# Optimization experiments

Measured on AMD Instinct MI355X. Metric: run time of the kernel, lower is better.

Reference implementation:

```python
import jax, jax.numpy as jnp
import numpy as np
from jax import lax

# --- block geometry (matches init_kwargs) ---
B = 8
DIM = 192
HEADS = 6
KEY_DIM = DIM // HEADS  # 32, attn_ratio=1 so d == key_dim and dh == DIM
HX, WX = 32, 32         # search region
HZ, WZ = 16, 16         # template region
T = 1                   # template_number
L = HX * WX + T * HZ * WZ  # 1280 tokens
MLP_HIDDEN = int(DIM * 4.0)
BN_EPS = 1e-5


def _build_bias_idx():
    """Replicates Attention.__init__ global_att=True bias-index construction.
    Unique-offset ids may be permuted vs torch dict-insertion order, which is an
    equivalent reparameterization of the (randomly initialized) bias table."""
    g = np.stack(np.meshgrid(np.arange(HX), np.arange(WX), indexing='ij'), -1).reshape(-1, 2)
    pts = [g]
    for i in range(T):
        r = np.arange(HX + HZ * i, WX + WZ * (i + 1))
        g2 = np.stack(np.meshgrid(r, r, indexing='ij'), -1).reshape(-1, 2)
        pts.append(g2)
    p = np.concatenate(pts, 0)                      # (L, 2)
    off = np.abs(p[:, None, :] - p[None, :, :])     # (L, L, 2)
    key = off[:, :, 0].astype(np.int64) * 4096 + off[:, :, 1]
    uniq, inv = np.unique(key, return_inverse=True)
    return inv.reshape(L, L).astype(np.int32), int(len(uniq))


def setup_inputs() -> dict:
    key = jax.random.key(0)
    ks = jax.random.split(key, 16)
    idx_np, n_off = _build_bias_idx()
    s = 0.02
    return {
        'xz': jax.random.normal(ks[0], (B, L, DIM), jnp.float32),
        'bias_idx': jnp.asarray(idx_np),
        'ln1_g': jnp.ones((DIM,), jnp.float32),
        'ln1_b': jnp.zeros((DIM,), jnp.float32),
        'wqkv': jax.random.normal(ks[1], (DIM, 3 * DIM), jnp.float32) * s,
        'bqkv': jnp.zeros((3 * DIM,), jnp.float32),
        'wproj': jax.random.normal(ks[2], (DIM, DIM), jnp.float32) * s,
        'bproj': jnp.zeros((DIM,), jnp.float32),
        'bias_table': jax.random.normal(ks[3], (HEADS, n_off), jnp.float32) * 0.1,
        'conv_w': jax.random.normal(ks[4], (3, 3, 1, DIM), jnp.float32) * 0.1,  # depthwise HWIO
        'bn_scale': jnp.ones((DIM,), jnp.float32) + jax.random.normal(ks[5], (DIM,), jnp.float32) * 0.01,
        'bn_bias': jax.random.normal(ks[6], (DIM,), jnp.float32) * 0.01,
        'ln2_g': jnp.ones((DIM,), jnp.float32),
        'ln2_b': jnp.zeros((DIM,), jnp.float32),
        'w1': jax.random.normal(ks[7], (DIM, MLP_HIDDEN), jnp.float32) * s,
        'b1': jnp.zeros((MLP_HIDDEN,), jnp.float32),
        'w2': jax.random.normal(ks[8], (MLP_HIDDEN, DIM), jnp.float32) * s,
        'b2': jnp.zeros((DIM,), jnp.float32),
    }


def _layernorm(x, g, b, eps=1e-5):
    mu = jnp.mean(x, -1, keepdims=True)
    var = jnp.mean(jnp.square(x - mu), -1, keepdims=True)
    return (x - mu) * lax.rsqrt(var + eps) * g + b


def reference(xz, bias_idx, ln1_g, ln1_b, wqkv, bqkv, wproj, bproj, bias_table,
              conv_w, bn_scale, bn_bias, ln2_g, ln2_b, w1, b1, w2, b2):
    Bn, N, D = xz.shape
    scale = KEY_DIM ** -0.5
    # --- Attention (LeViT-style with gathered relative-position bias) ---
    h = _layernorm(xz, ln1_g, ln1_b)
    qkv = (h @ wqkv + bqkv).reshape(Bn, N, HEADS, 3 * KEY_DIM)
    q, k, v = jnp.split(qkv, 3, axis=3)            # each (B, N, H, key_dim)
    bias = bias_table[:, bias_idx]                  # (H, N, N) gather
    attn = jnp.einsum('bnhd,bmhd->bhnm', q, k) * scale + bias
    attn = jax.nn.softmax(attn, axis=-1)
    o = jnp.einsum('bhnm,bmhd->bnhd', attn, v).reshape(Bn, N, D)
    xm = xz + o @ wproj + bproj
    # --- depthwise local conv (Conv2d_BN, BN folded to scale/bias) per segment ---
    segs = []
    start = 0
    for (Hh, Ww) in [(HX, WX)] + [(HZ, WZ)] * T:
        xc = xm[:, start:start + Hh * Ww, :].reshape(Bn, Hh, Ww, D)
        xc = lax.conv_general_dilated(
            xc, conv_w, window_strides=(1, 1), padding='SAME',
            dimension_numbers=('NHWC', 'HWIO', 'NHWC'), feature_group_count=D)
        xc = xc * bn_scale + bn_bias
        segs.append(xc.reshape(Bn, Hh * Ww, D))
        start += Hh * Ww
    xm = jnp.concatenate(segs, axis=1)
    # --- MLP with pre-LN (exact GELU, matching nn.GELU default) ---
    m = _layernorm(xm, ln2_g, ln2_b)
    m = jax.nn.gelu(m @ w1 + b1, approximate=False) @ w2 + b2
    return xm + m
```

## Files before the change

kernel.cpp:

```cpp
#include <hip/hip_runtime.h>
#include <hip/hip_bf16.h>

#define BATCH 8
#define LTOK 1280
#define DIMC 192
#define HEADS 6
#define KD 32
#define HID 768
#define NROWS (BATCH*LTOK)

typedef short s16x8 __attribute__((ext_vector_type(8)));
typedef float f32x4 __attribute__((ext_vector_type(4)));
typedef unsigned short u16;

#define QS (0.17677669529663687f * 1.4426950408889634f)
#define L2E 1.4426950408889634f

__device__ __forceinline__ u16 f2bf(float x) {
    unsigned u = __float_as_uint(x);
    u = (u + 0x7FFFu + ((u >> 16) & 1u)) >> 16;
    return (u16)u;
}
__device__ __forceinline__ float bflo(unsigned u) { return __uint_as_float(u << 16); }
__device__ __forceinline__ float bfhi(unsigned u) { return __uint_as_float(u & 0xffff0000u); }
__device__ __forceinline__ float fexp2(float x) { float r; asm("v_exp_f32 %0, %1" : "=v"(r) : "v"(x)); return r; }
__device__ __forceinline__ float frcp(float x)  { float r; asm("v_rcp_f32 %0, %1" : "=v"(r) : "v"(x)); return r; }

__global__ __launch_bounds__(256) void ln_kernel(const float* __restrict__ x,
                                                 const float* __restrict__ g,
                                                 const float* __restrict__ b,
                                                 u16* __restrict__ y) {
    int row = blockIdx.x * 4 + (threadIdx.x >> 6);
    int lane = threadIdx.x & 63;
    const float* xr = x + (size_t)row * DIMC;
    float v0 = xr[lane], v1 = xr[lane + 64], v2 = xr[lane + 128];
    float s = v0 + v1 + v2;
    float ss = v0 * v0 + v1 * v1 + v2 * v2;
    #pragma unroll
    for (int off = 32; off; off >>= 1) {
        s  += __shfl_xor(s, off);
        ss += __shfl_xor(ss, off);
    }
    float mu  = s * (1.0f / DIMC);
    float var = ss * (1.0f / DIMC) - mu * mu;
    float inv = rsqrtf(var + 1e-5f);
    u16* yr = y + (size_t)row * DIMC;
    yr[lane]       = f2bf((v0 - mu) * inv * g[lane]       + b[lane]);
    yr[lane + 64]  = f2bf((v1 - mu) * inv * g[lane + 64]  + b[lane + 64]);
    yr[lane + 128] = f2bf((v2 - mu) * inv * g[lane + 128] + b[lane + 128]);
}

__global__ __launch_bounds__(256) void pre_kernel(const float* w0, const float* w1,
                                                  const float* w2, const float* w3,
                                                  u16* o0, u16* o1, u16* o2, u16* o3,
                                                  const int* __restrict__ bidx,
                                                  const float* __restrict__ btab,
                                                  int n_off, u16* __restrict__ bm) {
    __shared__ float s[16][17];
    int f = blockIdx.x;
    if (f >= 1728) {
        size_t flat = (size_t)(f - 1728) * 1024 + (size_t)threadIdx.x * 4;
        int4 iv = *(const int4*)(bidx + flat);
        #pragma unroll
        for (int h = 0; h < HEADS; ++h) {
            const float* tab = btab + (size_t)h * n_off;
            ushort4 o;
            o.x = f2bf(tab[iv.x] * L2E);
            o.y = f2bf(tab[iv.y] * L2E);
            o.z = f2bf(tab[iv.z] * L2E);
            o.w = f2bf(tab[iv.w] * L2E);
            *(ushort4*)(bm + (size_t)h * (LTOK * LTOK) + flat) = o;
        }
        return;
    }
    const float* in; u16* out; int K, N, tn, tk;
    if (f < 432)       { in = w0; out = o0; K = 192; N = 576; int r = f;        tn = r % 36; tk = r / 36; }
    else if (f < 576)  { in = w1; out = o1; K = 192; N = 192; int r = f - 432;  tn = r % 12; tk = r / 12; }
    else if (f < 1152) { in = w2; out = o2; K = 192; N = 768; int r = f - 576;  tn = r % 48; tk = r / 48; }
    else               { in = w3; out = o3; K = 768; N = 192; int r = f - 1152; tn = r % 12; tk = r / 12; }
    int tx = threadIdx.x & 15, ty = threadIdx.x >> 4;
    s[ty][tx] = in[(size_t)(tk * 16 + ty) * N + tn * 16 + tx];
    __syncthreads();
    out[(size_t)(tn * 16 + ty) * K + tk * 16 + tx] = f2bf(s[tx][ty]);
}

template<int ACT, int RES, int OBF, int QKV, int K, int MTILE>
__global__ __launch_bounds__(256) void gemm_mfma(const u16* __restrict__ A,
                                                 const u16* __restrict__ Wt,
                                                 const float* __restrict__ bias,
                                                 const float* __restrict__ R,
                                                 void* __restrict__ Cp,
                                                 u16* __restrict__ qb,
                                                 u16* __restrict__ kp,
                                                 u16* __restrict__ vp,
                                                 int N) {
    constexpr int SUB = MTILE / 64;
    int tid = threadIdx.x;
    int L = tid & 63, w = tid >> 6;
    int r = L & 15, g = L >> 4;
    int m0 = blockIdx.y * MTILE + w * (16 * SUB);
    int n0 = blockIdx.x * 64;

    f32x4 acc[SUB][4] = {};
    const u16* Ab = A + (size_t)(m0 + r) * K + g * 8;
    const u16* Wb = Wt + (size_t)(n0 + r) * K + g * 8;
    #pragma unroll 6
    for (int k0 = 0; k0 < K; k0 += 32) {
        s16x8 af[SUB];
        #pragma unroll
        for (int mi = 0; mi < SUB; ++mi)
            af[mi] = *(const s16x8*)(Ab + (size_t)mi * 16 * K + k0);
        #pragma unroll
        for (int nn = 0; nn < 4; ++nn) {
            s16x8 bf = *(const s16x8*)(Wb + (size_t)nn * 16 * K + k0);
            #pragma unroll
            for (int mi = 0; mi < SUB; ++mi)
                acc[mi][nn] = __builtin_amdgcn_mfma_f32_16x16x32_bf16(af[mi], bf, acc[mi][nn], 0, 0, 0);
        }
    }

    #pragma unroll
    for (int mi = 0; mi < SUB; ++mi)
    #pragma unroll
    for (int nn = 0; nn < 4; ++nn) {
        int cb = n0 + nn * 16;
        #pragma unroll
        for (int i = 0; i < 4; ++i) {
            int row = m0 + mi * 16 + g * 4 + i;
            float v = acc[mi][nn][i] + bias[cb + r];
            if (QKV) {
                int h  = cb / 96, c0 = cb % 96;
                int reg = c0 >> 5;
                if (reg == 0) {
                    v *= QS;
                    qb[(size_t)row * DIMC + h * 32 + (c0 & 31) + r] = f2bf(v);
                } else {
                    int b_ = row / LTOK, t = row - b_ * LTOK;
                    int T = t >> 5, it = t & 31;
                    int d = (c0 & 31) + r;
                    if (reg == 1) {
                        int which = (it >> 2) & 1;
                        int ik = ((it >> 3) << 2) | (it & 3);
                        int Lk = ((d >> 3) << 4) + ik;
                        kp[((size_t)(b_ * HEADS + h) * 40 + T) * 1024 + which * 512 + Lk * 8 + (d & 7)] = f2bf(v);
                    } else {
                        int Lv = ((it >> 3) << 4) + (d & 15);
                        vp[((size_t)(b_ * HEADS + h) * 40 + T) * 1024 + (d >> 4) * 512 + Lv * 8 + (it & 7)] = f2bf(v);
                    }
                }
            } else {
                if (ACT == 1) {
                    float u = v;
                    float y = 0.7978845608028654f * (u + 0.044715f * u * u * u);
                    float e2 = fexp2(y * 2.885390081777927f);
                    v = u - u * frcp(e2 + 1.0f);
                }
                if (RES) v += R[(size_t)row * N + cb + r];
                if (OBF) ((u16*)Cp)[(size_t)row * N + cb + r] = f2bf(v);
                else     ((float*)Cp)[(size_t)row * N + cb + r] = v;
            }
        }
    }
}

__global__ __launch_bounds__(256) void attn_mfma(const u16* __restrict__ qb,
                                                 const u16* __restrict__ kp,
                                                 const u16* __restrict__ vp,
                                                 const u16* __restrict__ bm,
                                                 u16* __restrict__ ob) {
    __shared__ __align__(16) u16 kvs[2][2][2][1024];
    int tid = threadIdx.x;
    int L = tid & 63, w = tid >> 6;
    int r = L & 15, g = L >> 4;
    int L8 = L * 8;

    int bid = blockIdx.x;
    int work = (bid & 7) * 60 + (bid >> 3);
    int bp = work & 3;
    int hq = work >> 2;
    int qt = (hq % 20) * 4 + w;
    int h  = hq / 20;
    int b0 = bp * 2;

    s16x8 qfr[2];
    qfr[0] = *(const s16x8*)(qb + (size_t)(b0 * LTOK + qt * 16 + r) * DIMC + h * 32 + g * 8);
    qfr[1] = *(const s16x8*)(qb + (size_t)((b0 + 1) * LTOK + qt * 16 + r) * DIMC + h * 32 + g * 8);

    int sbi = w >> 1, skv = w & 1;
    const u16* gsrc = (skv ? vp : kp) + ((size_t)((b0 + sbi) * HEADS + h) * 40) * 1024 + L8;
    u16* lds0 = &kvs[0][sbi][skv][L8];
    u16* lds1 = &kvs[1][sbi][skv][L8];

    const u16* bmr = bm + ((size_t)h * LTOK + qt * 16 + r) * LTOK + g * 8;

    f32x4 acc0[2] = {}, acc1[2] = {};
    float lsum[2] = {0.f, 0.f};

    int4 sA = *(const int4*)(gsrc);
    int4 sB = *(const int4*)(gsrc + 512);
    int4 bvn = *(const int4*)(bmr);
    *(int4*)lds0 = sA;
    *(int4*)(lds0 + 512) = sB;
    __syncthreads();

    #pragma unroll 1
    for (int T = 0; T < 40; ++T) {
        int buf = T & 1;
        if (T < 39) {
            sA = *(const int4*)(gsrc + (size_t)(T + 1) * 1024);
            sB = *(const int4*)(gsrc + (size_t)(T + 1) * 1024 + 512);
        }
        int4 bv = bvn;
        if (T < 39) bvn = *(const int4*)(bmr + (size_t)(T + 1) * 32);

        f32x4 z0, z1;
        z0[0] = bflo(bv.x); z0[1] = bfhi(bv.x); z0[2] = bflo(bv.y); z0[3] = bfhi(bv.y);
        z1[0] = bflo(bv.z); z1[1] = bfhi(bv.z); z1[2] = bflo(bv.w); z1[3] = bfhi(bv.w);

        #pragma unroll
        for (int bi = 0; bi < 2; ++bi) {
            s16x8 kf0 = *(const s16x8*)&kvs[buf][bi][0][L8];
            s16x8 kf1 = *(const s16x8*)&kvs[buf][bi][0][512 + L8];
            f32x4 s0 = __builtin_amdgcn_mfma_f32_16x16x32_bf16(kf0, qfr[bi], z0, 0, 0, 0);
            f32x4 s1 = __builtin_amdgcn_mfma_f32_16x16x32_bf16(kf1, qfr[bi], z1, 0, 0, 0);
            float p[8];
            #pragma unroll
            for (int j = 0; j < 4; ++j) p[j] = fexp2(s0[j]);
            #pragma unroll
            for (int j = 0; j < 4; ++j) p[4 + j] = fexp2(s1[j]);
            lsum[bi] += ((p[0] + p[1]) + (p[2] + p[3])) + ((p[4] + p[5]) + (p[6] + p[7]));
            union { unsigned u[4]; s16x8 v; } pbu;
            #pragma unroll
            for (int j = 0; j < 4; ++j)
                asm("v_cvt_pk_bf16_f32 %0, %1, %2" : "=v"(pbu.u[j]) : "v"(p[2 * j]), "v"(p[2 * j + 1]));
            s16x8 v0 = *(const s16x8*)&kvs[buf][bi][1][L8];
            s16x8 v1 = *(const s16x8*)&kvs[buf][bi][1][512 + L8];
            acc0[bi] = __builtin_amdgcn_mfma_f32_16x16x32_bf16(pbu.v, v0, acc0[bi], 0, 0, 0);
            acc1[bi] = __builtin_amdgcn_mfma_f32_16x16x32_bf16(pbu.v, v1, acc1[bi], 0, 0, 0);
        }

        if (T < 39) {
            u16* ld = (T & 1) ? lds0 : lds1;
            *(int4*)ld = sA;
            *(int4*)(ld + 512) = sB;
        }
        __syncthreads();
    }

    #pragma unroll
    for (int bi = 0; bi < 2; ++bi) {
        float lr = lsum[bi];
        lr += __shfl_xor(lr, 16);
        lr += __shfl_xor(lr, 32);
        int b = b0 + bi;
        #pragma unroll
        for (int i = 0; i < 4; ++i) {
            float linv = frcp(__shfl(lr, 4 * g + i));
            size_t orow = (size_t)(b * LTOK + qt * 16 + 4 * g + i) * DIMC + h * 32 + r;
            ob[orow]      = f2bf(acc0[bi][i] * linv);
            ob[orow + 16] = f2bf(acc1[bi][i] * linv);
        }
    }
}

__global__ __launch_bounds__(256) void conv_bn_kernel(const float* __restrict__ xm,
                                                      const float* __restrict__ w,
                                                      const float* __restrict__ scale,
                                                      const float* __restrict__ bias,
                                                      float* __restrict__ out) {
    int idx = blockIdx.x * 256 + threadIdx.x;
    int cc = idx % 48, p = idx / 48;
    int c = cc * 4;
    int b = p / LTOK, t = p - b * LTOK;
    int H, W, base, y, x;
    if (t < 1024) { H = 32; W = 32; base = 0;    y = t >> 5;            x = t & 31; }
    else          { H = 16; W = 16; base = 1024; int tt = t - 1024; y = tt >> 4; x = tt & 15; }
    float4 acc = {0.f, 0.f, 0.f, 0.f};
    #pragma unroll
    for (int ky = 0; ky < 3; ++ky) {
        int yy = y + ky - 1;
        if (yy < 0 || yy >= H) continue;
        #pragma unroll
        for (int kx = 0; kx < 3; ++kx) {
            int xx = x + kx - 1;
            if (xx < 0 || xx >= W) continue;
            float4 wv = *(const float4*)(w + (ky * 3 + kx) * DIMC + c);
            float4 xv = *(const float4*)(xm + (size_t)(b * LTOK + base + yy * W + xx) * DIMC + c);
            acc.x += wv.x * xv.x; acc.y += wv.y * xv.y;
            acc.z += wv.z * xv.z; acc.w += wv.w * xv.w;
        }
    }
    float4 sv = *(const float4*)(scale + c);
    float4 bv = *(const float4*)(bias + c);
    float4 o;
    o.x = acc.x * sv.x + bv.x; o.y = acc.y * sv.y + bv.y;
    o.z = acc.z * sv.z + bv.z; o.w = acc.w * sv.w + bv.w;
    *(float4*)(out + (size_t)(b * LTOK + t) * DIMC + c) = o;
}

extern "C" void kernel_launch(void* const* d_in, const int* in_sizes, int n_in,
                              void* d_out, int out_size, void* d_ws, size_t ws_size,
                              hipStream_t stream) {
    const float* xz       = (const float*)d_in[0];
    const int*   bidx     = (const int*)  d_in[1];
    const float* ln1_g    = (const float*)d_in[2];
    const float* ln1_b    = (const float*)d_in[3];
    const float* wqkv     = (const float*)d_in[4];
    const float* bqkv     = (const float*)d_in[5];
    const float* wproj    = (const float*)d_in[6];
    const float* bproj    = (const float*)d_in[7];
    const float* btab     = (const float*)d_in[8];
    const float* conv_w   = (const float*)d_in[9];
    const float* bn_scale = (const float*)d_in[10];
    const float* bn_bias  = (const float*)d_in[11];
    const float* ln2_g    = (const float*)d_in[12];
    const float* ln2_b    = (const float*)d_in[13];
    const float* w1       = (const float*)d_in[14];
    const float* b1       = (const float*)d_in[15];
    const float* w2       = (const float*)d_in[16];
    const float* b2       = (const float*)d_in[17];
    int n_off = in_sizes[8] / HEADS;
    float* out = (float*)d_out;

    char* wsb = (char*)d_ws;
    u16*  hbuf   = (u16*)(wsb + 0);
    u16*  ob     = (u16*)(wsb + 0);
    u16*  wqkvT  = (u16*)(wsb + 3932160);
    u16*  wprojT = (u16*)(wsb + 4153344);
    u16*  w1T    = (u16*)(wsb + 4227072);
    u16*  w2T    = (u16*)(wsb + 4521984);
    u16*  bm     = (u16*)(wsb + 4816896);
    u16*  hid    = (u16*)(wsb + 4816896);
    u16*  kp     = (u16*)(wsb + 24477696);
    u16*  vp     = (u16*)(wsb + 28409856);
    float* xm2   = (float*)(wsb + 24477696);
    u16*  qb     = (u16*)(wsb + 32342016);
    float* xm    = (float*)(wsb + 32342016);

    pre_kernel<<<1728 + LTOK * LTOK / 1024, 256, 0, stream>>>(
        wqkv, wproj, w1, w2, wqkvT, wprojT, w1T, w2T, bidx, btab, n_off, bm);
    ln_kernel<<<NROWS / 4, 256, 0, stream>>>(xz, ln1_g, ln1_b, hbuf);
    gemm_mfma<0,0,0,1,DIMC,128><<<dim3(576 / 64, NROWS / 128), 256, 0, stream>>>(
        hbuf, wqkvT, bqkv, nullptr, nullptr, qb, kp, vp, 3 * DIMC);
    attn_mfma<<<480, 256, 0, stream>>>(qb, kp, vp, bm, ob);
    gemm_mfma<0,1,0,0,DIMC,64><<<dim3(DIMC / 64, NROWS / 64), 256, 0, stream>>>(
        ob, wprojT, bproj, xz, xm, nullptr, nullptr, nullptr, DIMC);
    conv_bn_kernel<<<NROWS * 48 / 256, 256, 0, stream>>>(xm, conv_w, bn_scale, bn_bias, xm2);
    ln_kernel<<<NROWS / 4, 256, 0, stream>>>(xm2, ln2_g, ln2_b, hbuf);
    gemm_mfma<1,0,1,0,DIMC,128><<<dim3(HID / 64, NROWS / 128), 256, 0, stream>>>(
        hbuf, w1T, b1, nullptr, hid, nullptr, nullptr, nullptr, HID);
    gemm_mfma<0,1,0,0,HID,128><<<dim3(DIMC / 64, NROWS / 128), 256, 0, stream>>>(
        hid, w2T, b2, xm2, out, nullptr, nullptr, nullptr, DIMC);
}
```

Measured before the change: 143.4 us.

## Fuse layernorm into QKV and MLP GEMMs, split attention per batch

Folds the LayerNorm gamma into the pre-transposed bf16 weights and beta into a precomputed effective bias. The QKV and first MLP GEMMs now read fp32 activations and normalize in their prologue, which removes two standalone LN kernels and their bf16 intermediate round trips. Attention blocks now each handle a single batch instead of a pair, doubling the grid and halving the LDS staging per block. The folded biases are stored temporarily in the output buffer, which relies on the final GEMM overwriting it later.

Result: slower. 155.3 us (+8.3%).

```diff
diff --git a/kernel.cpp b/kernel.cpp
--- a/kernel.cpp
+++ b/kernel.cpp
@@ -26,38 +26,34 @@
 __device__ __forceinline__ float fexp2(float x) { float r; asm("v_exp_f32 %0, %1" : "=v"(r) : "v"(x)); return r; }
 __device__ __forceinline__ float frcp(float x)  { float r; asm("v_rcp_f32 %0, %1" : "=v"(r) : "v"(x)); return r; }
 
-__global__ __launch_bounds__(256) void ln_kernel(const float* __restrict__ x,
-                                                 const float* __restrict__ g,
-                                                 const float* __restrict__ b,
-                                                 u16* __restrict__ y) {
-    int row = blockIdx.x * 4 + (threadIdx.x >> 6);
-    int lane = threadIdx.x & 63;
-    const float* xr = x + (size_t)row * DIMC;
-    float v0 = xr[lane], v1 = xr[lane + 64], v2 = xr[lane + 128];
-    float s = v0 + v1 + v2;
-    float ss = v0 * v0 + v1 * v1 + v2 * v2;
-    #pragma unroll
-    for (int off = 32; off; off >>= 1) {
-        s  += __shfl_xor(s, off);
-        ss += __shfl_xor(ss, off);
-    }
-    float mu  = s * (1.0f / DIMC);
-    float var = ss * (1.0f / DIMC) - mu * mu;
-    float inv = rsqrtf(var + 1e-5f);
-    u16* yr = y + (size_t)row * DIMC;
-    yr[lane]       = f2bf((v0 - mu) * inv * g[lane]       + b[lane]);
-    yr[lane + 64]  = f2bf((v1 - mu) * inv * g[lane + 64]  + b[lane + 64]);
-    yr[lane + 128] = f2bf((v2 - mu) * inv * g[lane + 128] + b[lane + 128]);
-}
-
 __global__ __launch_bounds__(256) void pre_kernel(const float* w0, const float* w1,
                                                   const float* w2, const float* w3,
                                                   u16* o0, u16* o1, u16* o2, u16* o3,
                                                   const int* __restrict__ bidx,
                                                   const float* __restrict__ btab,
-                                                  int n_off, u16* __restrict__ bm) {
+                                                  int n_off, u16* __restrict__ bm,
+                                                  const float* ln1g, const float* ln1b,
+                                                  const float* ln2g, const float* ln2b,
+                                                  const float* bqkv, const float* b1,
+                                                  float* bqf, float* b1f) {
     __shared__ float s[16][17];
+    __shared__ float rb[4][64];
     int f = blockIdx.x;
+    if (f >= 3328) {
+        int f2 = f - 3328;
+        const float* W; const float* beta; const float* bb; float* outb; int N, n0;
+        if (f2 < 9) { W = w0; beta = ln1b; bb = bqkv; outb = bqf; N = 576; n0 = f2 * 64; }
+        else        { W = w2; beta = ln2b; bb = b1;   outb = b1f; N = 768; n0 = (f2 - 9) * 64; }
+        int col = threadIdx.x & 63, seg = threadIdx.x >> 6;
+        float p = 0.f;
+        for (int k = seg * 48; k < seg * 48 + 48; ++k)
+            p += beta[k] * W[(size_t)k * N + n0 + col];
+        rb[seg][col] = p;
+        __syncthreads();
+        if (seg == 0)
+            outb[n0 + col] = bb[n0 + col] + rb[0][col] + rb[1][col] + rb[2][col] + rb[3][col];
+        return;
+    }
     if (f >= 1728) {
         size_t flat = (size_t)(f - 1728) * 1024 + (size_t)threadIdx.x * 4;
         int4 iv = *(const int4*)(bidx + flat);
@@ -73,26 +69,24 @@
         }
         return;
     }
-    const float* in; u16* out; int K, N, tn, tk;
-    if (f < 432)       { in = w0; out = o0; K = 192; N = 576; int r = f;        tn = r % 36; tk = r / 36; }
-    else if (f < 576)  { in = w1; out = o1; K = 192; N = 192; int r = f - 432;  tn = r % 12; tk = r / 12; }
-    else if (f < 1152) { in = w2; out = o2; K = 192; N = 768; int r = f - 576;  tn = r % 48; tk = r / 48; }
-    else               { in = w3; out = o3; K = 768; N = 192; int r = f - 1152; tn = r % 12; tk = r / 12; }
+    const float* in; u16* out; const float* gam; int K, N, tn, tk;
+    if (f < 432)       { in = w0; out = o0; gam = ln1g; K = 192; N = 576; int r = f;        tn = r % 36; tk = r / 36; }
+    else if (f < 576)  { in = w1; out = o1; gam = nullptr; K = 192; N = 192; int r = f - 432;  tn = r % 12; tk = r / 12; }
+    else if (f < 1152) { in = w2; out = o2; gam = ln2g; K = 192; N = 768; int r = f - 576;  tn = r % 48; tk = r / 48; }
+    else               { in = w3; out = o3; gam = nullptr; K = 768; N = 192; int r = f - 1152; tn = r % 12; tk = r / 12; }
     int tx = threadIdx.x & 15, ty = threadIdx.x >> 4;
     s[ty][tx] = in[(size_t)(tk * 16 + ty) * N + tn * 16 + tx];
     __syncthreads();
-    out[(size_t)(tn * 16 + ty) * K + tk * 16 + tx] = f2bf(s[tx][ty]);
-}
-
-template<int ACT, int RES, int OBF, int QKV, int K, int MTILE>
+    float gs = gam ? gam[tk * 16 + tx] : 1.0f;
+    out[(size_t)(tn * 16 + ty) * K + tk * 16 + tx] = f2bf(s[tx][ty] * gs);
+}
+
+template<int ACT, int RES, int OBF, int K, int MTILE>
 __global__ __launch_bounds__(256) void gemm_mfma(const u16* __restrict__ A,
                                                  const u16* __restrict__ Wt,
                                                  const float* __restrict__ bias,
                                                  const float* __restrict__ R,
                                                  void* __restrict__ Cp,
-                                                 u16* __restrict__ qb,
-                                                 u16* __restrict__ kp,
-                                                 u16* __restrict__ vp,
                                                  int N) {
     constexpr int SUB = MTILE / 64;
     int tid = threadIdx.x;
@@ -128,6 +122,81 @@
         for (int i = 0; i < 4; ++i) {
             int row = m0 + mi * 16 + g * 4 + i;
             float v = acc[mi][nn][i] + bias[cb + r];
+            if (ACT == 1) {
+                float u = v;
+                float y = 0.7978845608028654f * (u + 0.044715f * u * u * u);
+                float e2 = fexp2(y * 2.885390081777927f);
+                v = u - u * frcp(e2 + 1.0f);
+            }
+            if (RES) v += R[(size_t)row * N + cb + r];
+            if (OBF) ((u16*)Cp)[(size_t)row * N + cb + r] = f2bf(v);
+            else     ((float*)Cp)[(size_t)row * N + cb + r] = v;
+        }
+    }
+}
+
+template<int ACT, int QKV>
+__global__ __launch_bounds__(256) void gemm_ln_mfma(const float* __restrict__ A,
+                                                    const u16* __restrict__ Wt,
+                                                    const float* __restrict__ biasf,
+                                                    void* __restrict__ Cp,
+                                                    u16* __restrict__ qb,
+                                                    u16* __restrict__ kp,
+                                                    u16* __restrict__ vp,
+                                                    int N) {
+    constexpr int K = 192;
+    int tid = threadIdx.x;
+    int L = tid & 63, w = tid >> 6;
+    int r = L & 15, g = L >> 4;
+    int m0 = blockIdx.y * 64 + w * 16;
+    int n0 = blockIdx.x * 64;
+
+    const float* Ar = A + (size_t)(m0 + r) * K;
+    float4 xv[12];
+    #pragma unroll
+    for (int kk = 0; kk < 6; ++kk) {
+        xv[2 * kk]     = *(const float4*)(Ar + kk * 32 + g * 8);
+        xv[2 * kk + 1] = *(const float4*)(Ar + kk * 32 + g * 8 + 4);
+    }
+    float s = 0.f, ss = 0.f;
+    #pragma unroll
+    for (int i = 0; i < 12; ++i) {
+        s  += xv[i].x + xv[i].y + xv[i].z + xv[i].w;
+        ss += xv[i].x * xv[i].x + xv[i].y * xv[i].y + xv[i].z * xv[i].z + xv[i].w * xv[i].w;
+    }
+    s  += __shfl_xor(s, 16);  s  += __shfl_xor(s, 32);
+    ss += __shfl_xor(ss, 16); ss += __shfl_xor(ss, 32);
+    float mu  = s * (1.0f / K);
+    float var = ss * (1.0f / K) - mu * mu;
+    float inv = rsqrtf(var + 1e-5f);
+
+    s16x8 af[6];
+    #pragma unroll
+    for (int kk = 0; kk < 6; ++kk) {
+        float vs[8] = {xv[2*kk].x, xv[2*kk].y, xv[2*kk].z, xv[2*kk].w,
+                       xv[2*kk+1].x, xv[2*kk+1].y, xv[2*kk+1].z, xv[2*kk+1].w};
+        #pragma unroll
+        for (int j = 0; j < 8; ++j) af[kk][j] = (short)f2bf((vs[j] - mu) * inv);
+    }
+
+    f32x4 acc[4] = {};
+    const u16* Wb = Wt + (size_t)(n0 + r) * K + g * 8;
+    #pragma unroll
+    for (int kk = 0; kk < 6; ++kk) {
+        #pragma unroll
+        for (int nn = 0; nn < 4; ++nn) {
+            s16x8 bf = *(const s16x8*)(Wb + (size_t)nn * 16 * K + kk * 32);
+            acc[nn] = __builtin_amdgcn_mfma_f32_16x16x32_bf16(af[kk], bf, acc[nn], 0, 0, 0);
+        }
+    }
+
+    #pragma unroll
+    for (int nn = 0; nn < 4; ++nn) {
+        int cb = n0 + nn * 16;
+        #pragma unroll
+        for (int i = 0; i < 4; ++i) {
+            int row = m0 + g * 4 + i;
+            float v = acc[nn][i] + biasf[cb + r];
             if (QKV) {
                 int h  = cb / 96, c0 = cb % 96;
                 int reg = c0 >> 5;
@@ -155,9 +224,7 @@
                     float e2 = fexp2(y * 2.885390081777927f);
                     v = u - u * frcp(e2 + 1.0f);
                 }
-                if (RES) v += R[(size_t)row * N + cb + r];
-                if (OBF) ((u16*)Cp)[(size_t)row * N + cb + r] = f2bf(v);
-                else     ((float*)Cp)[(size_t)row * N + cb + r] = v;
+                ((u16*)Cp)[(size_t)row * N + cb + r] = f2bf(v);
             }
         }
     }
@@ -168,48 +235,40 @@
                                                  const u16* __restrict__ vp,
                                                  const u16* __restrict__ bm,
                                                  u16* __restrict__ ob) {
-    __shared__ __align__(16) u16 kvs[2][2][2][1024];
+    __shared__ __align__(16) u16 kvs[2][2][1024];
     int tid = threadIdx.x;
     int L = tid & 63, w = tid >> 6;
     int r = L & 15, g = L >> 4;
     int L8 = L * 8;
 
     int bid = blockIdx.x;
-    int work = (bid & 7) * 60 + (bid >> 3);
-    int bp = work & 3;
-    int hq = work >> 2;
+    int work = (bid & 7) * 120 + (bid >> 3);
+    int b  = work & 7;
+    int hq = work >> 3;
     int qt = (hq % 20) * 4 + w;
     int h  = hq / 20;
-    int b0 = bp * 2;
-
-    s16x8 qfr[2];
-    qfr[0] = *(const s16x8*)(qb + (size_t)(b0 * LTOK + qt * 16 + r) * DIMC + h * 32 + g * 8);
-    qfr[1] = *(const s16x8*)(qb + (size_t)((b0 + 1) * LTOK + qt * 16 + r) * DIMC + h * 32 + g * 8);
-
-    int sbi = w >> 1, skv = w & 1;
-    const u16* gsrc = (skv ? vp : kp) + ((size_t)((b0 + sbi) * HEADS + h) * 40) * 1024 + L8;
-    u16* lds0 = &kvs[0][sbi][skv][L8];
-    u16* lds1 = &kvs[1][sbi][skv][L8];
+
+    s16x8 qf = *(const s16x8*)(qb + (size_t)(b * LTOK + qt * 16 + r) * DIMC + h * 32 + g * 8);
+
+    int skv = w >> 1, half = w & 1;
+    const u16* gsrc = (skv ? vp : kp) + (size_t)(b * HEADS + h) * 40 * 1024 + half * 512 + L8;
+    u16* d0 = &kvs[0][skv][half * 512 + L8];
+    u16* d1 = &kvs[1][skv][half * 512 + L8];
 
     const u16* bmr = bm + ((size_t)h * LTOK + qt * 16 + r) * LTOK + g * 8;
 
-    f32x4 acc0[2] = {}, acc1[2] = {};
-    float lsum[2] = {0.f, 0.f};
+    f32x4 acc0 = {0.f, 0.f, 0.f, 0.f}, acc1 = {0.f, 0.f, 0.f, 0.f};
+    float lsum = 0.f;
 
     int4 sA = *(const int4*)(gsrc);
-    int4 sB = *(const int4*)(gsrc + 512);
     int4 bvn = *(const int4*)(bmr);
-    *(int4*)lds0 = sA;
-    *(int4*)(lds0 + 512) = sB;
+    *(int4*)d0 = sA;
     __syncthreads();
 
     #pragma unroll 1
     for (int T = 0; T < 40; ++T) {
         int buf = T & 1;
-        if (T < 39) {
-            sA = *(const int4*)(gsrc + (size_t)(T + 1) * 1024);
-            sB = *(const int4*)(gsrc + (size_t)(T + 1) * 1024 + 512);
-        }
+        if (T < 39) sA = *(const int4*)(gsrc + (size_t)(T + 1) * 1024);
         int4 bv = bvn;
         if (T < 39) bvn = *(const int4*)(bmr + (size_t)(T + 1) * 32);
 
@@ -217,49 +276,38 @@
         z0[0] = bflo(bv.x); z0[1] = bfhi(bv.x); z0[2] = bflo(bv.y); z0[3] = bfhi(bv.y);
         z1[0] = bflo(bv.z); z1[1] = bfhi(bv.z); z1[2] = bflo(bv.w); z1[3] = bfhi(bv.w);
 
-        #pragma unroll
-        for (int bi = 0; bi < 2; ++bi) {
-            s16x8 kf0 = *(const s16x8*)&kvs[buf][bi][0][L8];
-            s16x8 kf1 = *(const s16x8*)&kvs[buf][bi][0][512 + L8];
-            f32x4 s0 = __builtin_amdgcn_mfma_f32_16x16x32_bf16(kf0, qfr[bi], z0, 0, 0, 0);
-            f32x4 s1 = __builtin_amdgcn_mfma_f32_16x16x32_bf16(kf1, qfr[bi], z1, 0, 0, 0);
-            float p[8];
-            #pragma unroll
-            for (int j = 0; j < 4; ++j) p[j] = fexp2(s0[j]);
-            #pragma unroll
-            for (int j = 0; j < 4; ++j) p[4 + j] = fexp2(s1[j]);
-            lsum[bi] += ((p[0] + p[1]) + (p[2] + p[3])) + ((p[4] + p[5]) + (p[6] + p[7]));
-            union { unsigned u[4]; s16x8 v; } pbu;
-            #pragma unroll
-            for (int j = 0; j < 4; ++j)
-                asm("v_cvt_pk_bf16_f32 %0, %1, %2" : "=v"(pbu.u[j]) : "v"(p[2 * j]), "v"(p[2 * j + 1]));
-            s16x8 v0 = *(const s16x8*)&kvs[buf][bi][1][L8];
-            s16x8 v1 = *(const s16x8*)&kvs[buf][bi][1][512 + L8];
-            acc0[bi] = __builtin_amdgcn_mfma_f32_16x16x32_bf16(pbu.v, v0, acc0[bi], 0, 0, 0);
-            acc1[bi] = __builtin_amdgcn_mfma_f32_16x16x32_bf16(pbu.v, v1, acc1[bi], 0, 0, 0);
-        }
-
-        if (T < 39) {
-            u16* ld = (T & 1) ? lds0 : lds1;
-            *(int4*)ld = sA;
-            *(int4*)(ld + 512) = sB;
-        }
+        s16x8 kf0 = *(const s16x8*)&kvs[buf][0][L8];
+        s16x8 kf1 = *(const s16x8*)&kvs[buf][0][512 + L8];
+        f32x4 s0 = __builtin_amdgcn_mfma_f32_16x16x32_bf16(kf0, qf, z0, 0, 0, 0);
+        f32x4 s1 = __builtin_amdgcn_mfma_f32_16x16x32_bf16(kf1, qf, z1, 0, 0, 0);
+        float p[8];
+        #pragma unroll
+        for (int j = 0; j < 4; ++j) p[j] = fexp2(s0[j]);
+        #pragma unroll
+        for (int j = 0; j < 4; ++j) p[4 + j] = fexp2(s1[j]);
+        lsum += ((p[0] + p[1]) + (p[2] + p[3])) + ((p[4] + p[5]) + (p[6] + p[7]));
+        union { unsigned u[4]; s16x8 v; } pbu;
+        #pragma unroll
+        for (int j = 0; j < 4; ++j)
+            asm("v_cvt_pk_bf16_f32 %0, %1, %2" : "=v"(pbu.u[j]) : "v"(p[2 * j]), "v"(p[2 * j + 1]));
+        s16x8 v0 = *(const s16x8*)&kvs[buf][1][L8];
+        s16x8 v1 = *(const s16x8*)&kvs[buf][1][512 + L8];
+        acc0 = __builtin_amdgcn_mfma_f32_16x16x32_bf16(pbu.v, v0, acc0, 0, 0, 0);
+        acc1 = __builtin_amdgcn_mfma_f32_16x16x32_bf16(pbu.v, v1, acc1, 0, 0, 0);
+
+        if (T < 39) *(int4*)((T & 1) ? d0 : d1) = sA;
         __syncthreads();
     }
 
-    #pragma unroll
-    for (int bi = 0; bi < 2; ++bi) {
-        float lr = lsum[bi];
-        lr += __shfl_xor(lr, 16);
-        lr += __shfl_xor(lr, 32);
-        int b = b0 + bi;
-        #pragma unroll
-        for (int i = 0; i < 4; ++i) {
-            float linv = frcp(__shfl(lr, 4 * g + i));
-            size_t orow = (size_t)(b * LTOK + qt * 16 + 4 * g + i) * DIMC + h * 32 + r;
-            ob[orow]      = f2bf(acc0[bi][i] * linv);
-            ob[orow + 16] = f2bf(acc1[bi][i] * linv);
-        }
+    float lr = lsum;
+    lr += __shfl_xor(lr, 16);
+    lr += __shfl_xor(lr, 32);
+    #pragma unroll
+    for (int i = 0; i < 4; ++i) {
+        float linv = frcp(__shfl(lr, 4 * g + i));
+        size_t orow = (size_t)(b * LTOK + qt * 16 + 4 * g + i) * DIMC + h * 32 + r;
+        ob[orow]      = f2bf(acc0[i] * linv);
+        ob[orow + 16] = f2bf(acc1[i] * linv);
     }
 }
 
@@ -323,7 +371,6 @@
     float* out = (float*)d_out;
 
     char* wsb = (char*)d_ws;
-    u16*  hbuf   = (u16*)(wsb + 0);
     u16*  ob     = (u16*)(wsb + 0);
     u16*  wqkvT  = (u16*)(wsb + 3932160);
     u16*  wprojT = (u16*)(wsb + 4153344);
@@ -336,19 +383,20 @@
     float* xm2   = (float*)(wsb + 24477696);
     u16*  qb     = (u16*)(wsb + 32342016);
     float* xm    = (float*)(wsb + 32342016);
-
-    pre_kernel<<<1728 + LTOK * LTOK / 1024, 256, 0, stream>>>(
-        wqkv, wproj, w1, w2, wqkvT, wprojT, w1T, w2T, bidx, btab, n_off, bm);
-    ln_kernel<<<NROWS / 4, 256, 0, stream>>>(xz, ln1_g, ln1_b, hbuf);
-    gemm_mfma<0,0,0,1,DIMC,128><<<dim3(576 / 64, NROWS / 128), 256, 0, stream>>>(
-        hbuf, wqkvT, bqkv, nullptr, nullptr, qb, kp, vp, 3 * DIMC);
-    attn_mfma<<<480, 256, 0, stream>>>(qb, kp, vp, bm, ob);
-    gemm_mfma<0,1,0,0,DIMC,64><<<dim3(DIMC / 64, NROWS / 64), 256, 0, stream>>>(
-        ob, wprojT, bproj, xz, xm, nullptr, nullptr, nullptr, DIMC);
+    float* bqf = (float*)d_out;
+    float* b1f = (float*)d_out + 576;
+
+    pre_kernel<<<3349, 256, 0, stream>>>(
+        wqkv, wproj, w1, w2, wqkvT, wprojT, w1T, w2T, bidx, btab, n_off, bm,
+        ln1_g, ln1_b, ln2_g, ln2_b, bqkv, b1, bqf, b1f);
+    gemm_ln_mfma<0,1><<<dim3(9, 160), 256, 0, stream>>>(
+        xz, wqkvT, bqf, nullptr, qb, kp, vp, 3 * DIMC);
+    attn_mfma<<<960, 256, 0, stream>>>(qb, kp, vp, bm, ob);
+    gemm_mfma<0,1,0,DIMC,64><<<dim3(3, 160), 256, 0, stream>>>(
+        ob, wprojT, bproj, xz, xm, DIMC);
     conv_bn_kernel<<<NROWS * 48 / 256, 256, 0, stream>>>(xm, conv_w, bn_scale, bn_bias, xm2);
-    ln_kernel<<<NROWS / 4, 256, 0, stream>>>(xm2, ln2_g, ln2_b, hbuf);
-    gemm_mfma<1,0,1,0,DIMC,128><<<dim3(HID / 64, NROWS / 128), 256, 0, stream>>>(
-        hbuf, w1T, b1, nullptr, hid, nullptr, nullptr, nullptr, HID);
-    gemm_mfma<0,1,0,0,HID,128><<<dim3(DIMC / 64, NROWS / 128), 256, 0, stream>>>(
-        hid, w2T, b2, xm2, out, nullptr, nullptr, nullptr, DIMC);
-}
+    gemm_ln_mfma<1,0><<<dim3(12, 160), 256, 0, stream>>>(
+        xm2, w1T, b1f, hid, nullptr, nullptr, nullptr, HID);
+    gemm_mfma<0,1,0,HID,128><<<dim3(3, 80), 256, 0, stream>>>(
+        hid, w2T, b2, xm2, out, DIMC);
+}
```
